# Performance work log

Hardware: AMD Instinct MI355X
Metric: run time of the kernel (lower is better)

The kernel has to match this reference:

```python
import jax, jax.numpy as jnp
import numpy as np

ROPE_BASE = 10000.0

def rotate_half(x):
    d = x.shape[-1] // 2
    return jnp.concatenate([-x[..., d:], x[..., :d]], axis=-1)

def rope_cos_sin(seq_len, head_dim, dtype=jnp.float32):
    inv_freq = 1.0 / (ROPE_BASE ** (jnp.arange(0, head_dim, 2, dtype=jnp.float32) / head_dim))
    t = jnp.arange(seq_len, dtype=jnp.float32)
    freqs = jnp.outer(t, inv_freq)              # [T, hd/2]
    emb = jnp.concatenate([freqs, freqs], axis=-1)  # [T, hd]
    return jnp.cos(emb).astype(dtype), jnp.sin(emb).astype(dtype)

def alibi_slopes(num_heads):
    return jnp.asarray([2.0 ** (-8.0 * i / num_heads) for i in range(1, num_heads + 1)], dtype=jnp.float32)

def setup_inputs() -> dict:
    key = jax.random.key(0)
    k1, k2, k3 = jax.random.split(key, 3)
    B, T, H = 2, 2048, 1024
    return {
        "q": jax.random.normal(k1, (B, T, H), dtype=jnp.float32),
        "k": jax.random.normal(k2, (B, T, H), dtype=jnp.float32),
        "v": jax.random.normal(k3, (B, T, H), dtype=jnp.float32),
        "num_heads": 16,
    }

def reference(q, k, v, num_heads):
    B, T, H = q.shape
    nh = num_heads
    hd = H // nh
    q = q.reshape(B, T, nh, hd)
    k = k.reshape(B, T, nh, hd)
    v = v.reshape(B, T, nh, hd)
    cos, sin = rope_cos_sin(T, hd, q.dtype)      # [T, hd]
    cos = cos[None, :, None, :]                  # [1, T, 1, hd]
    sin = sin[None, :, None, :]
    q = q * cos + rotate_half(q) * sin
    k = k * cos + rotate_half(k) * sin
    # ALiBi additive bias: [nh, T, T]
    rel = jnp.arange(T)[None, :] - jnp.arange(T)[:, None]   # memory - context
    bias = alibi_slopes(nh)[:, None, None] * rel.astype(q.dtype)
    scale = 1.0 / jnp.sqrt(jnp.asarray(hd, dtype=q.dtype))
    scores = jnp.einsum('bqhd,bkhd->bhqk', q, k) * scale + bias[None]
    attn = jax.nn.softmax(scores, axis=-1)
    out = jnp.einsum('bhqk,bkhd->bqhd', attn, v)
    return out.reshape(B, T, H)
```

## Files before the change

kernel.cpp:

```cpp
#include <hip/hip_runtime.h>
#include <math.h>

#define TB 2
#define TT 2048
#define NH 16
#define HD 64
#define HSZ 1024

typedef float floatx4 __attribute__((ext_vector_type(4)));
typedef __bf16 bf16x4 __attribute__((ext_vector_type(4)));
typedef __bf16 bf16x8 __attribute__((ext_vector_type(8)));

#define LOG2E  1.4426950408889634f
#define NEGF   (-0.4152410118609203f)
#define INV2PI 0.15915494309189535f

__global__ __launch_bounds__(256)
void prep_kernel(const float* __restrict__ K, const float* __restrict__ V,
                 __bf16* __restrict__ Kp, __bf16* __restrict__ Vp) {
    int blk = blockIdx.x;
    int kt = blk & 31;
    int bh = blk >> 5;
    int b = bh >> 4, h = bh & 15;
    int tid = threadIdx.x;

    {
        int key = tid >> 2, qq = tid & 3;
        int tglob = kt * 64 + key;
        const float* krow = K + ((size_t)(b * TT + tglob)) * HSZ + h * HD + qq * 8;
        float x0[8], x1[8];
        *(floatx4*)&x0[0] = *(const floatx4*)&krow[0];
        *(floatx4*)&x0[4] = *(const floatx4*)&krow[4];
        *(floatx4*)&x1[0] = *(const floatx4*)&krow[32];
        *(floatx4*)&x1[4] = *(const floatx4*)&krow[36];
        bf16x8 y0, y1;
        #pragma unroll
        for (int j = 0; j < 8; ++j) {
            float freq = exp2f((float)(qq * 8 + j) * NEGF);
            float rv = (float)tglob * freq * INV2PI;
            rv -= floorf(rv);
            float s = __builtin_amdgcn_sinf(rv);
            float c = __builtin_amdgcn_cosf(rv);
            y0[j] = (__bf16)(x0[j] * c - x1[j] * s);
            y1[j] = (__bf16)(x1[j] * c + x0[j] * s);
        }
        size_t base = ((size_t)blk * 4 + (key & 3)) * 1024 + (size_t)(qq * 16 + (key >> 2)) * 8;
        *(bf16x8*)(Kp + base)       = y0;
        *(bf16x8*)(Kp + base + 512) = y1;
    }

    __shared__ __bf16 lt[64][72];
    {
        int vkey = tid >> 2, dg = (tid & 3) * 16;
        const float* vrow = V + ((size_t)(b * TT + kt * 64 + vkey)) * HSZ + h * HD + dg;
        floatx4 v0 = *(const floatx4*)&vrow[0];
        floatx4 v1 = *(const floatx4*)&vrow[4];
        floatx4 v2 = *(const floatx4*)&vrow[8];
        floatx4 v3 = *(const floatx4*)&vrow[12];
        #pragma unroll
        for (int j = 0; j < 4; ++j) {
            lt[dg + j][vkey]      = (__bf16)v0[j];
            lt[dg + 4 + j][vkey]  = (__bf16)v1[j];
            lt[dg + 8 + j][vkey]  = (__bf16)v2[j];
            lt[dg + 12 + j][vkey] = (__bf16)v3[j];
        }
    }
    __syncthreads();
    #pragma unroll
    for (int ss = 0; ss < 2; ++ss) {
        int s = tid + ss * 256;
        int hg = s >> 6;
        int l = s & 63;
        int lq = l >> 4, lr = l & 15;
        int h2 = hg >> 2, g = hg & 3;
        bf16x8 o = *(const bf16x8*)&lt[g * 16 + lr][h2 * 32 + lq * 8];
        *(bf16x8*)(Vp + (size_t)blk * 4096 + (size_t)hg * 512 + (size_t)l * 8) = o;
    }
}

__global__ __launch_bounds__(256, 2)
void attn_kernel(const float* __restrict__ Q, const __bf16* __restrict__ Kp,
                 const __bf16* __restrict__ Vp, float* __restrict__ Out) {
    int blk0 = blockIdx.x;
    int blk = (blk0 & 7) * 64 + (blk0 >> 3);

    int qb = blk & 15;
    int bh = blk >> 4;
    int b = bh >> 4, h = bh & 15;
    int tid = threadIdx.x;
    int wave = tid >> 6, lane = tid & 63;
    int lane15 = lane & 15, quad = lane >> 4;

    __shared__ __align__(16) __bf16 sP[4][2][16][72];

    const float scale2 = 0.125f * LOG2E;
    const float slope2 = exp2f(-0.5f * (float)(h + 1)) * LOG2E;
    const float ms     = slope2 * 2047.0f + 20.0f;

    int qbase = qb * 128 + wave * 32;
    int d0 = quad * 8;
    bf16x8 aQ0[2], aQ1[2];
    #pragma unroll
    for (int qf = 0; qf < 2; ++qf) {
        int t_q = qbase + qf * 16 + lane15;
        const float* qrow = Q + ((size_t)(b * TT + t_q) * HSZ) + h * HD;
        float q0[8], q1[8];
        *(floatx4*)&q0[0] = *(const floatx4*)&qrow[d0];
        *(floatx4*)&q0[4] = *(const floatx4*)&qrow[d0 + 4];
        *(floatx4*)&q1[0] = *(const floatx4*)&qrow[d0 + 32];
        *(floatx4*)&q1[4] = *(const floatx4*)&qrow[d0 + 36];
        #pragma unroll
        for (int j = 0; j < 8; ++j) {
            float freq = exp2f((float)(d0 + j) * NEGF);
            float rv = (float)t_q * freq * INV2PI;
            rv -= floorf(rv);
            float sn = __builtin_amdgcn_sinf(rv);
            float cs = __builtin_amdgcn_cosf(rv);
            aQ0[qf][j] = (__bf16)((q0[j] * cs - q1[j] * sn) * scale2);
            aQ1[qf][j] = (__bf16)((q1[j] * cs + q0[j] * sn) * scale2);
        }
    }

    float slk2[4];
    #pragma unroll
    for (int nt = 0; nt < 4; ++nt)
        slk2[nt] = slope2 * (float)(4 * lane15 + nt) - ms;
    const float dstep = slope2 * 64.0f;

    floatx4 O[2][4];
    float lrow[2][4];
    #pragma unroll
    for (int qf = 0; qf < 2; ++qf)
        #pragma unroll
        for (int r = 0; r < 4; ++r) {
            O[qf][r] = (floatx4){0.f, 0.f, 0.f, 0.f};
            lrow[qf][r] = 0.f;
        }

    const __bf16* Kb = Kp + (size_t)bh * (TT * HD) + (size_t)lane * 8;
    const __bf16* Vb = Vp + (size_t)bh * (TT * HD) + (size_t)lane * 8;

    const int kt1 = TT / 64;

    bf16x8 bk[4][2];
    {
        const __bf16* kbase = Kb;
        #pragma unroll
        for (int nt = 0; nt < 4; ++nt) {
            bk[nt][0] = *(const bf16x8*)(kbase + nt * 1024);
            bk[nt][1] = *(const bf16x8*)(kbase + nt * 1024 + 512);
        }
    }

    #pragma unroll 1
    for (int kt = 0; kt < kt1; ++kt) {
        const __bf16* vbase = Vb + (size_t)kt * 4096;
        bf16x8 bv[2][4];
        #pragma unroll
        for (int hg = 0; hg < 8; ++hg)
            bv[hg >> 2][hg & 3] = *(const bf16x8*)(vbase + hg * 512);

        float biask = dstep * (float)kt;
        #pragma unroll
        for (int qf = 0; qf < 2; ++qf) {
            float P[4][4];
            #pragma unroll
            for (int nt = 0; nt < 4; ++nt) {
                floatx4 acc = {0.f, 0.f, 0.f, 0.f};
                acc = __builtin_amdgcn_mfma_f32_16x16x32_bf16(aQ0[qf], bk[nt][0], acc, 0, 0, 0);
                acc = __builtin_amdgcn_mfma_f32_16x16x32_bf16(aQ1[qf], bk[nt][1], acc, 0, 0, 0);
                float bias = slk2[nt] + biask;
                #pragma unroll
                for (int r = 0; r < 4; ++r)
                    P[nt][r] = __builtin_amdgcn_exp2f(acc[r] + bias);
            }
            #pragma unroll
            for (int r = 0; r < 4; ++r) {
                lrow[qf][r] += (P[0][r] + P[1][r]) + (P[2][r] + P[3][r]);
                bf16x4 pp;
                pp[0] = (__bf16)P[0][r]; pp[1] = (__bf16)P[1][r];
                pp[2] = (__bf16)P[2][r]; pp[3] = (__bf16)P[3][r];
                *(bf16x4*)&sP[wave][qf][quad * 4 + r][4 * lane15] = pp;
            }
        }

        if (kt + 1 < kt1) {
            const __bf16* kbase = Kb + (size_t)(kt + 1) * 4096;
            #pragma unroll
            for (int nt = 0; nt < 4; ++nt) {
                bk[nt][0] = *(const bf16x8*)(kbase + nt * 1024);
                bk[nt][1] = *(const bf16x8*)(kbase + nt * 1024 + 512);
            }
        }

        #pragma unroll
        for (int qf = 0; qf < 2; ++qf) {
            #pragma unroll
            for (int h2 = 0; h2 < 2; ++h2) {
                bf16x8 aP = *(const bf16x8*)&sP[wave][qf][lane15][h2 * 32 + quad * 8];
                O[qf][0] = __builtin_amdgcn_mfma_f32_16x16x32_bf16(aP, bv[h2][0], O[qf][0], 0, 0, 0);
                O[qf][1] = __builtin_amdgcn_mfma_f32_16x16x32_bf16(aP, bv[h2][1], O[qf][1], 0, 0, 0);
                O[qf][2] = __builtin_amdgcn_mfma_f32_16x16x32_bf16(aP, bv[h2][2], O[qf][2], 0, 0, 0);
                O[qf][3] = __builtin_amdgcn_mfma_f32_16x16x32_bf16(aP, bv[h2][3], O[qf][3], 0, 0, 0);
            }
        }
    }

    #pragma unroll
    for (int qf = 0; qf < 2; ++qf) {
        #pragma unroll
        for (int r = 0; r < 4; ++r) {
            float l = lrow[qf][r];
            l += __shfl_xor(l, 1);
            l += __shfl_xor(l, 2);
            l += __shfl_xor(l, 4);
            l += __shfl_xor(l, 8);
            float inv = 1.0f / l;
            int t = qbase + qf * 16 + quad * 4 + r;
            size_t base = ((size_t)(b * TT + t)) * HSZ + h * HD + lane15;
            Out[base +  0] = O[qf][0][r] * inv;
            Out[base + 16] = O[qf][1][r] * inv;
            Out[base + 32] = O[qf][2][r] * inv;
            Out[base + 48] = O[qf][3][r] * inv;
        }
    }
}

extern "C" void kernel_launch(void* const* d_in, const int* in_sizes, int n_in,
                              void* d_out, int out_size, void* d_ws, size_t ws_size,
                              hipStream_t stream) {
    const float* q = (const float*)d_in[0];
    const float* k = (const float*)d_in[1];
    const float* v = (const float*)d_in[2];
    float* out = (float*)d_out;

    char* ws = (char*)d_ws;
    __bf16* Kp = (__bf16*)ws;
    __bf16* Vp = (__bf16*)(ws + (size_t)8 * 1024 * 1024);

    prep_kernel<<<dim3(TB * NH * (TT / 64)), 256, 0, stream>>>(k, v, Kp, Vp);
    attn_kernel<<<dim3(TB * NH * 16), 256, 0, stream>>>(q, Kp, Vp, out);
}
```

Measured before the change: 136.9 us.

## Stage K/V tiles through double-buffered LDS with async global_load_lds

Each wave previously loaded its own copy of the K and V fragments straight from global memory into registers. Now the block cooperatively copies each 64-key K/V tile into a double-buffered LDS region with global_load_lds, prefetching the next tile while the current one is computed. This removes the 4x redundant global traffic across waves, at the cost of LDS reads, extra LDS capacity, and a block-wide barrier per iteration. It also adds s_setprio around the MFMA sections and swizzles the prep kernel's block order.

```diff
diff --git a/kernel.cpp b/kernel.cpp
--- a/kernel.cpp
+++ b/kernel.cpp
@@ -18,7 +18,8 @@
 __global__ __launch_bounds__(256)
 void prep_kernel(const float* __restrict__ K, const float* __restrict__ V,
                  __bf16* __restrict__ Kp, __bf16* __restrict__ Vp) {
-    int blk = blockIdx.x;
+    int blk0 = blockIdx.x;
+    int blk = ((blk0 & 7) << 7) + (blk0 >> 3);
     int kt = blk & 31;
     int bh = blk >> 5;
     int b = bh >> 4, h = bh & 15;
@@ -91,6 +92,7 @@
     int wave = tid >> 6, lane = tid & 63;
     int lane15 = lane & 15, quad = lane >> 4;
 
+    __shared__ __align__(16) unsigned char kvbuf[2][16384];
     __shared__ __align__(16) __bf16 sP[4][2][16][72];
 
     const float scale2 = 0.125f * LOG2E;
@@ -137,33 +139,56 @@
             lrow[qf][r] = 0.f;
         }
 
-    const __bf16* Kb = Kp + (size_t)bh * (TT * HD) + (size_t)lane * 8;
-    const __bf16* Vb = Vp + (size_t)bh * (TT * HD) + (size_t)lane * 8;
+    const __bf16* KpT = Kp + (size_t)bh * (TT * HD);
+    const __bf16* VpT = Vp + (size_t)bh * (TT * HD);
+
+    auto stage = [&](int buf, int kt_) {
+        const unsigned char* gk = (const unsigned char*)(KpT + (size_t)kt_ * 4096);
+        const unsigned char* gv = (const unsigned char*)(VpT + (size_t)kt_ * 4096);
+        unsigned char* lb = &kvbuf[buf][0];
+        int wl = wave * 1024 + lane * 16;
+        int wb = wave * 1024;
+        #pragma unroll
+        for (int c = 0; c < 2; ++c) {
+            __builtin_amdgcn_global_load_lds(
+                (const __attribute__((address_space(1))) unsigned int*)(gk + c * 4096 + wl),
+                (__attribute__((address_space(3))) unsigned int*)(lb + c * 4096 + wb),
+                16, 0, 0);
+            __builtin_amdgcn_global_load_lds(
+                (const __attribute__((address_space(1))) unsigned int*)(gv + c * 4096 + wl),
+                (__attribute__((address_space(3))) unsigned int*)(lb + 8192 + c * 4096 + wb),
+                16, 0, 0);
+        }
+    };
+
+    stage(0, 0);
+    __syncthreads();
 
     const int kt1 = TT / 64;
-
-    bf16x8 bk[4][2];
-    {
-        const __bf16* kbase = Kb;
-        #pragma unroll
-        for (int nt = 0; nt < 4; ++nt) {
-            bk[nt][0] = *(const bf16x8*)(kbase + nt * 1024);
-            bk[nt][1] = *(const bf16x8*)(kbase + nt * 1024 + 512);
-        }
-    }
 
     #pragma unroll 1
     for (int kt = 0; kt < kt1; ++kt) {
-        const __bf16* vbase = Vb + (size_t)kt * 4096;
+        int cur = kt & 1;
+        if (kt + 1 < kt1) stage(cur ^ 1, kt + 1);
+
+        const unsigned char* kb = &kvbuf[cur][0];
+
+        bf16x8 bk[4][2];
+        #pragma unroll
+        for (int nt = 0; nt < 4; ++nt) {
+            bk[nt][0] = *(const bf16x8*)(kb + nt * 2048 + lane * 16);
+            bk[nt][1] = *(const bf16x8*)(kb + nt * 2048 + 1024 + lane * 16);
+        }
         bf16x8 bv[2][4];
         #pragma unroll
         for (int hg = 0; hg < 8; ++hg)
-            bv[hg >> 2][hg & 3] = *(const bf16x8*)(vbase + hg * 512);
+            bv[hg >> 2][hg & 3] = *(const bf16x8*)(kb + 8192 + hg * 1024 + lane * 16);
 
         float biask = dstep * (float)kt;
         #pragma unroll
         for (int qf = 0; qf < 2; ++qf) {
             float P[4][4];
+            __builtin_amdgcn_s_setprio(1);
             #pragma unroll
             for (int nt = 0; nt < 4; ++nt) {
                 floatx4 acc = {0.f, 0.f, 0.f, 0.f};
@@ -174,6 +199,7 @@
                 for (int r = 0; r < 4; ++r)
                     P[nt][r] = __builtin_amdgcn_exp2f(acc[r] + bias);
             }
+            __builtin_amdgcn_s_setprio(0);
             #pragma unroll
             for (int r = 0; r < 4; ++r) {
                 lrow[qf][r] += (P[0][r] + P[1][r]) + (P[2][r] + P[3][r]);
@@ -184,26 +210,21 @@
             }
         }
 
-        if (kt + 1 < kt1) {
-            const __bf16* kbase = Kb + (size_t)(kt + 1) * 4096;
-            #pragma unroll
-            for (int nt = 0; nt < 4; ++nt) {
-                bk[nt][0] = *(const bf16x8*)(kbase + nt * 1024);
-                bk[nt][1] = *(const bf16x8*)(kbase + nt * 1024 + 512);
-            }
-        }
-
         #pragma unroll
         for (int qf = 0; qf < 2; ++qf) {
             #pragma unroll
             for (int h2 = 0; h2 < 2; ++h2) {
                 bf16x8 aP = *(const bf16x8*)&sP[wave][qf][lane15][h2 * 32 + quad * 8];
+                __builtin_amdgcn_s_setprio(1);
                 O[qf][0] = __builtin_amdgcn_mfma_f32_16x16x32_bf16(aP, bv[h2][0], O[qf][0], 0, 0, 0);
                 O[qf][1] = __builtin_amdgcn_mfma_f32_16x16x32_bf16(aP, bv[h2][1], O[qf][1], 0, 0, 0);
                 O[qf][2] = __builtin_amdgcn_mfma_f32_16x16x32_bf16(aP, bv[h2][2], O[qf][2], 0, 0, 0);
                 O[qf][3] = __builtin_amdgcn_mfma_f32_16x16x32_bf16(aP, bv[h2][3], O[qf][3], 0, 0, 0);
+                __builtin_amdgcn_s_setprio(0);
             }
         }
+
+        __syncthreads();
     }
 
     #pragma unroll
```

New measurement: 143.7 us. +4.9%, slower.
